# Kernel optimization log

Hardware: AMD Instinct MI355X
Metric: run time of the kernel (lower is better)

Reference implementation:

```python
import jax, jax.numpy as jnp
import numpy as np
from itertools import permutations

NB_OBJ = 3
DIM_BODY = 10
DIM_OBJECT = 15
OBJ_IDS = np.array([[0, 1, 2], [3, 4, 5], [6, 7, 8]])
LOG_SIG_MIN, LOG_SIG_MAX = -20.0, 2.0


def _lin(key, fan_in, fan_out):
    # torch nn.Linear default init: U(-1/sqrt(fan_in), 1/sqrt(fan_in))
    kw, kb = jax.random.split(key)
    lim = 1.0 / np.sqrt(fan_in)
    w = jax.random.uniform(kw, (fan_in, fan_out), jnp.float32, -lim, lim)
    b = jax.random.uniform(kb, (fan_out,), jnp.float32, -lim, lim)
    return w, b


def setup_inputs() -> dict:
    key = jax.random.key(0)
    ks = jax.random.split(key, 8)
    B = 65536
    d_phi_in, hid, d_phi_out, d_act = 58, 256, 256, 4

    obs = jax.random.normal(ks[0], (B, DIM_BODY + NB_OBJ * DIM_OBJECT), jnp.float32)
    ag = jax.random.normal(ks[1], (B, 9), jnp.float32)
    g = jax.random.normal(ks[2], (B, 9), jnp.float32)

    phi_w1, phi_b1 = _lin(ks[3], d_phi_in, hid)
    phi_w2, phi_b2 = _lin(ks[4], hid, d_phi_out)
    rho_w1, rho_b1 = _lin(ks[5], d_phi_out, 256)
    mean_w, mean_b = _lin(ks[6], 256, d_act)
    logstd_w, logstd_b = _lin(ks[7], 256, d_act)

    return {
        "obs": obs, "ag": ag, "g": g,
        "phi_w1": phi_w1, "phi_b1": phi_b1,
        "phi_w2": phi_w2, "phi_b2": phi_b2,
        "rho_w1": rho_w1, "rho_b1": rho_b1,
        "mean_w": mean_w, "mean_b": mean_b,
        "logstd_w": logstd_w, "logstd_b": logstd_b,
    }


def reference(obs, ag, g, phi_w1, phi_b1, phi_w2, phi_b2,
              rho_w1, rho_b1, mean_w, mean_b, logstd_w, logstd_b):
    B = obs.shape[0]
    obs_body = obs[:, :DIM_BODY]                       # [B, 10]
    eye = jnp.eye(NB_OBJ, dtype=obs.dtype)
    # obs_objects[i]: [B, 3 one-hot + 15 features]
    obs_objects = [
        jnp.concatenate(
            [jnp.broadcast_to(eye[i], (B, NB_OBJ)),
             obs[:, DIM_BODY + DIM_OBJECT * i: DIM_BODY + DIM_OBJECT * (i + 1)]],
            axis=1)
        for i in range(NB_OBJ)
    ]
    perms = list(permutations(range(NB_OBJ), 2))       # 6 ordered pairs
    # inp: [6, B, 58]
    inp = jnp.stack([
        jnp.concatenate([ag[:, OBJ_IDS[i]], ag[:, OBJ_IDS[j]],
                         g[:, OBJ_IDS[i]], g[:, OBJ_IDS[j]],
                         obs_body, obs_objects[i], obs_objects[j]], axis=1)
        for i, j in perms
    ])
    # shared phi MLP over all pairs
    h = jax.nn.relu(inp @ phi_w1 + phi_b1)             # [6, B, 256]
    phi_out = jax.nn.relu(h @ phi_w2 + phi_b2)         # [6, B, 256]
    pooled = phi_out.sum(axis=0)                       # [B, 256] sum-pool over pairs
    # rho MLP
    x = jax.nn.relu(pooled @ rho_w1 + rho_b1)          # [B, 256]
    mean = x @ mean_w + mean_b                         # [B, 4]
    logstd = jnp.clip(x @ logstd_w + logstd_b, LOG_SIG_MIN, LOG_SIG_MAX)
    return mean, logstd
```

## Files before the change

### kernel.cpp

```cpp
#include <hip/hip_runtime.h>


typedef __bf16 bf16x8 __attribute__((ext_vector_type(8)));
typedef float f32x4 __attribute__((ext_vector_type(4)));
typedef unsigned short u16x8 __attribute__((ext_vector_type(8)));

#define HB_OFF   0
#define INP0_OFF 32768
#define INP1_OFF 40960
#define RAW_OFF  49152
#define STAB_OFF 59648
#define LDS_TOTAL 60416

__device__ __forceinline__ unsigned short f2bf(float f) {
  union { float f; unsigned u; } v; v.f = f;
  unsigned r = v.u + 0x7fffu + ((v.u >> 16) & 1u);
  return (unsigned short)(r >> 16);
}
__device__ __forceinline__ int swz512(int o) { return o ^ (((o >> 9) & 7) << 4); }
__device__ __forceinline__ int swz128(int o) { return o ^ (((o >> 7) & 7) << 4); }
__device__ __forceinline__ f32x4 mfma16(bf16x8 a, bf16x8 b, f32x4 c) {
  return __builtin_amdgcn_mfma_f32_16x16x32_bf16(a, b, c, 0, 0, 0);
}
__device__ __forceinline__ uint2 pack4(f32x4 v) {
  uint2 r;
  asm("v_cvt_pk_bf16_f32 %0, %1, %2" : "=v"(r.x) : "v"(v[0]), "v"(v[1]));
  asm("v_cvt_pk_bf16_f32 %0, %1, %2" : "=v"(r.y) : "v"(v[2]), "v"(v[3]));
  return r;
}

__global__ void actor_prep(const float* __restrict__ w1, const float* __restrict__ w2,
                           const float* __restrict__ rho, const float* __restrict__ mw,
                           const float* __restrict__ lw, unsigned short* __restrict__ ws16) {
  int idx = blockIdx.x * blockDim.x + threadIdx.x;
  const int T = 16384 + 65536 + 65536 + 4096;
  for (; idx < T; idx += gridDim.x * blockDim.x) {
    float v;
    if (idx < 16384) {
      int n = idx >> 6, k = idx & 63;
      v = (k < 58) ? w1[k * 256 + n] : 0.f;
    } else if (idx < 81920) {
      int o = idx - 16384; int n = o >> 8, k = o & 255;
      v = w2[k * 256 + n];
    } else if (idx < 147456) {
      int o = idx - 81920; int n = o >> 8, k = o & 255;
      v = rho[k * 256 + n];
    } else {
      int o = idx - 147456; int n = o >> 8, k = o & 255;
      v = (n < 4) ? mw[k * 4 + n] : ((n < 8) ? lw[k * 4 + (n - 4)] : 0.f);
    }
    ws16[idx] = f2bf(v);
  }
}

__global__ __launch_bounds__(512, 1) void actor_main(
    const float* __restrict__ obs, const float* __restrict__ ag, const float* __restrict__ g,
    const float* __restrict__ b1v, const float* __restrict__ b2v, const float* __restrict__ rbv,
    const float* __restrict__ mbv, const float* __restrict__ lbv,
    const unsigned short* __restrict__ ws16,
    float* __restrict__ out, int B) {
  __shared__ char smem[LDS_TOTAL];
  unsigned short* rawp = (unsigned short*)(smem + RAW_OFF);
  unsigned short* stab = (unsigned short*)(smem + STAB_OFF);

  const unsigned short* w1t   = ws16;
  const unsigned short* w2t   = ws16 + 16384;
  const unsigned short* rhot  = ws16 + 81920;
  const unsigned short* headt = ws16 + 147456;

  const int tid = threadIdx.x;
  const int lane = tid & 63;
  const int wv = tid >> 6;
  const int l15 = lane & 15;
  const int lq = lane >> 4;
  const int wbase = wv * 32;
  const int ntiles = B / 64;
  const f32x4 fzero = {0.f, 0.f, 0.f, 0.f};

  bf16x8 wf2[8][2];
#pragma unroll
  for (int kk = 0; kk < 8; kk++)
#pragma unroll
    for (int nt = 0; nt < 2; nt++)
      wf2[kk][nt] = *(const bf16x8*)&w2t[(wbase + nt * 16 + l15) * 256 + kk * 32 + lq * 8];
  bf16x8 w1r[2][2];
#pragma unroll
  for (int nt = 0; nt < 2; nt++)
#pragma unroll
    for (int kk = 0; kk < 2; kk++)
      w1r[nt][kk] = *(const bf16x8*)&w1t[(wbase + nt * 16 + l15) * 64 + kk * 32 + lq * 8];
  f32x4 b1f[2], b2f[2], rbf[2];
#pragma unroll
  for (int nt = 0; nt < 2; nt++) {
    b1f[nt] = *(const f32x4*)&b1v[wbase + nt * 16 + lq * 4];
    b2f[nt] = *(const f32x4*)&b2v[wbase + nt * 16 + lq * 4];
    rbf[nt] = *(const f32x4*)&rbv[wbase + nt * 16 + lq * 4];
  }
  f32x4 mb4 = *(const f32x4*)mbv;
  f32x4 lb4 = *(const f32x4*)lbv;

  if (tid < 384) {
    const int PI[6] = {0, 0, 1, 1, 2, 2};
    const int PJ[6] = {1, 2, 0, 2, 0, 1};
    int p = tid >> 6, c = tid & 63;
    int pi = PI[p], pj = PJ[p], s;
    if (c < 3)       s = 56 + 3 * pi + c;
    else if (c < 6)  s = 56 + 3 * pj + (c - 3);
    else if (c < 9)  s = 65 + 3 * pi + (c - 6);
    else if (c < 12) s = 65 + 3 * pj + (c - 9);
    else if (c < 22) s = c - 12;
    else if (c < 25) s = ((c - 22) == pi) ? 75 : 74;
    else if (c < 40) s = 10 + 15 * pi + (c - 25);
    else if (c < 43) s = ((c - 40) == pj) ? 75 : 74;
    else if (c < 58) s = 10 + 15 * pj + (c - 43);
    else             s = 74;
    stab[tid] = (unsigned short)s;
  }

  for (int t = blockIdx.x; t < ntiles; t += gridDim.x) {
    const long brow = (long)t * 64;

    for (int i = tid; i < 64 * 55; i += 512) {
      int r = i / 55, c = i - r * 55;
      rawp[r * 82 + c] = f2bf(obs[brow * 55 + i]);
    }
    for (int i = tid; i < 64 * 9; i += 512) {
      int r = i / 9, c = i - r * 9;
      rawp[r * 82 + 56 + c] = f2bf(ag[brow * 9 + i]);
      rawp[r * 82 + 65 + c] = f2bf(g[brow * 9 + i]);
    }
    if (tid < 64) {
      rawp[tid * 82 + 55] = 0;
      rawp[tid * 82 + 74] = 0;
      rawp[tid * 82 + 75] = 0x3F80;
    }
    __syncthreads();

    {
      int r = tid >> 3, oct = tid & 7;
      u16x8 sv = *(const u16x8*)&stab[0 * 64 + oct * 8];
      const unsigned short* rw = &rawp[r * 82];
      uint4 w;
      w.x = (unsigned)rw[sv[0]] | ((unsigned)rw[sv[1]] << 16);
      w.y = (unsigned)rw[sv[2]] | ((unsigned)rw[sv[3]] << 16);
      w.z = (unsigned)rw[sv[4]] | ((unsigned)rw[sv[5]] << 16);
      w.w = (unsigned)rw[sv[6]] | ((unsigned)rw[sv[7]] << 16);
      *(uint4*)(smem + INP0_OFF + swz128(r * 128 + oct * 16)) = w;
    }
    __syncthreads();

    f32x4 pooled[2][4];
#pragma unroll
    for (int a = 0; a < 2; a++)
#pragma unroll
      for (int b = 0; b < 4; b++) pooled[a][b] = fzero;

    for (int p = 0; p < 6; p++) {
      const int ib = (p & 1) ? INP1_OFF : INP0_OFF;
      f32x4 acc1[2][4];
#pragma unroll
      for (int nt = 0; nt < 2; nt++)
#pragma unroll
        for (int mt = 0; mt < 4; mt++) acc1[nt][mt] = b1f[nt];
#pragma unroll
      for (int kk = 0; kk < 2; kk++) {
        bf16x8 xf[4];
#pragma unroll
        for (int mt = 0; mt < 4; mt++)
          xf[mt] = *(const bf16x8*)(smem + ib +
                     swz128((mt * 16 + l15) * 128 + (kk * 32 + lq * 8) * 2));
#pragma unroll
        for (int nt = 0; nt < 2; nt++)
#pragma unroll
          for (int mt = 0; mt < 4; mt++)
            acc1[nt][mt] = mfma16(w1r[nt][kk], xf[mt], acc1[nt][mt]);
      }
#pragma unroll
      for (int nt = 0; nt < 2; nt++)
#pragma unroll
        for (int mt = 0; mt < 4; mt++) {
          f32x4 h;
#pragma unroll
          for (int r = 0; r < 4; r++) h[r] = fmaxf(acc1[nt][mt][r], 0.f);
          *(uint2*)(smem + HB_OFF + swz512((mt * 16 + l15) * 512 +
                     (wbase + nt * 16 + lq * 4) * 2)) = pack4(h);
        }
      __syncthreads();

      if (p < 5) {
        int r = tid >> 3, oct = tid & 7;
        u16x8 sv = *(const u16x8*)&stab[(p + 1) * 64 + oct * 8];
        const unsigned short* rw = &rawp[r * 82];
        uint4 w;
        w.x = (unsigned)rw[sv[0]] | ((unsigned)rw[sv[1]] << 16);
        w.y = (unsigned)rw[sv[2]] | ((unsigned)rw[sv[3]] << 16);
        w.z = (unsigned)rw[sv[4]] | ((unsigned)rw[sv[5]] << 16);
        w.w = (unsigned)rw[sv[6]] | ((unsigned)rw[sv[7]] << 16);
        *(uint4*)(smem + ((p & 1) ? INP0_OFF : INP1_OFF) + swz128(r * 128 + oct * 16)) = w;
      }
      f32x4 acc2[2][4];
#pragma unroll
      for (int nt = 0; nt < 2; nt++)
#pragma unroll
        for (int mt = 0; mt < 4; mt++) acc2[nt][mt] = b2f[nt];
      __builtin_amdgcn_s_setprio(1);
#pragma unroll
      for (int kk = 0; kk < 8; kk++) {
        bf16x8 hf[4];
#pragma unroll
        for (int mt = 0; mt < 4; mt++)
          hf[mt] = *(const bf16x8*)(smem + HB_OFF +
                     swz512((mt * 16 + l15) * 512 + (kk * 32 + lq * 8) * 2));
#pragma unroll
        for (int nt = 0; nt < 2; nt++)
#pragma unroll
          for (int mt = 0; mt < 4; mt++)
            acc2[nt][mt] = mfma16(wf2[kk][nt], hf[mt], acc2[nt][mt]);
      }
      __builtin_amdgcn_s_setprio(0);
#pragma unroll
      for (int nt = 0; nt < 2; nt++)
#pragma unroll
        for (int mt = 0; mt < 4; mt++)
#pragma unroll
          for (int r = 0; r < 4; r++)
            pooled[nt][mt][r] += fmaxf(acc2[nt][mt][r], 0.f);
      __syncthreads();
    }

#pragma unroll
    for (int nt = 0; nt < 2; nt++)
#pragma unroll
      for (int mt = 0; mt < 4; mt++)
        *(uint2*)(smem + HB_OFF + swz512((mt * 16 + l15) * 512 +
                   (wbase + nt * 16 + lq * 4) * 2)) = pack4(pooled[nt][mt]);
    __syncthreads();

    f32x4 acc3[2][4];
#pragma unroll
    for (int nt = 0; nt < 2; nt++)
#pragma unroll
      for (int mt = 0; mt < 4; mt++) acc3[nt][mt] = rbf[nt];
#pragma unroll
    for (int kk = 0; kk < 8; kk++) {
      bf16x8 wf[2], hf[4];
#pragma unroll
      for (int nt = 0; nt < 2; nt++)
        wf[nt] = *(const bf16x8*)&rhot[(wbase + nt * 16 + l15) * 256 + kk * 32 + lq * 8];
#pragma unroll
      for (int mt = 0; mt < 4; mt++)
        hf[mt] = *(const bf16x8*)(smem + HB_OFF +
                   swz512((mt * 16 + l15) * 512 + (kk * 32 + lq * 8) * 2));
#pragma unroll
      for (int nt = 0; nt < 2; nt++)
#pragma unroll
        for (int mt = 0; mt < 4; mt++)
          acc3[nt][mt] = mfma16(wf[nt], hf[mt], acc3[nt][mt]);
    }
    __syncthreads();
#pragma unroll
    for (int nt = 0; nt < 2; nt++)
#pragma unroll
      for (int mt = 0; mt < 4; mt++) {
        f32x4 x;
#pragma unroll
        for (int r = 0; r < 4; r++) x[r] = fmaxf(acc3[nt][mt][r], 0.f);
        *(uint2*)(smem + HB_OFF + swz512((mt * 16 + l15) * 512 +
                   (wbase + nt * 16 + lq * 4) * 2)) = pack4(x);
      }
    __syncthreads();

    if (wv < 4) {
      f32x4 acc4 = fzero;
      if (lq == 0)      acc4 = mb4;
      else if (lq == 1) acc4 = lb4;
#pragma unroll
      for (int kk = 0; kk < 8; kk++) {
        bf16x8 hf = *(const bf16x8*)(smem + HB_OFF +
                      swz512((wv * 16 + l15) * 512 + (kk * 32 + lq * 8) * 2));
        bf16x8 wf = *(const bf16x8*)&headt[l15 * 256 + kk * 32 + lq * 8];
        acc4 = mfma16(wf, hf, acc4);
      }
      long gr = brow + wv * 16 + l15;
      if (lq == 0) {
        *(f32x4*)&out[gr * 4] = acc4;
      } else if (lq == 1) {
        f32x4 u;
#pragma unroll
        for (int r = 0; r < 4; r++) u[r] = fminf(fmaxf(acc4[r], -20.f), 2.f);
        *(f32x4*)&out[(long)B * 4 + gr * 4] = u;
      }
    }
  }
}

extern "C" void kernel_launch(void* const* d_in, const int* in_sizes, int n_in,
                              void* d_out, int out_size, void* d_ws, size_t ws_size,
                              hipStream_t stream) {
  const float* obs = (const float*)d_in[0];
  const float* ag  = (const float*)d_in[1];
  const float* g   = (const float*)d_in[2];
  const float* w1  = (const float*)d_in[3];
  const float* b1  = (const float*)d_in[4];
  const float* w2  = (const float*)d_in[5];
  const float* b2  = (const float*)d_in[6];
  const float* rw  = (const float*)d_in[7];
  const float* rb  = (const float*)d_in[8];
  const float* mw  = (const float*)d_in[9];
  const float* mb  = (const float*)d_in[10];
  const float* lw  = (const float*)d_in[11];
  const float* lb  = (const float*)d_in[12];
  int B = in_sizes[0] / 55;

  unsigned short* ws16 = (unsigned short*)d_ws;
  hipLaunchKernelGGL(actor_prep, dim3(128), dim3(256), 0, stream, w1, w2, rw, mw, lw, ws16);
  hipLaunchKernelGGL(actor_main, dim3(256), dim3(512), 0, stream,
                     obs, ag, g, b1, b2, rb, mb, lb, ws16, (float*)d_out, B);
}
```

Baseline: 112.8 us.

## Double block size to 1024 threads, each wave computing 16 output columns

Launches 1024-thread blocks and assigns each of 16 waves a 16-column slice of every layer instead of 32 columns per wave across 8 waves. This halves per-wave register state (weights, accumulators, pooled sums) and raises the number of resident waves to hide LDS and MFMA latency. The launch bounds request of 4 blocks per CU may force a very small register budget and cause spills, and barriers now synchronize twice as many waves.

```diff
diff --git a/kernel.cpp b/kernel.cpp
--- a/kernel.cpp
+++ b/kernel.cpp
@@ -53,7 +53,7 @@
   }
 }
 
-__global__ __launch_bounds__(512, 1) void actor_main(
+__global__ __launch_bounds__(1024, 4) void actor_main(
     const float* __restrict__ obs, const float* __restrict__ ag, const float* __restrict__ g,
     const float* __restrict__ b1v, const float* __restrict__ b2v, const float* __restrict__ rbv,
     const float* __restrict__ mbv, const float* __restrict__ lbv,
@@ -73,29 +73,21 @@
   const int wv = tid >> 6;
   const int l15 = lane & 15;
   const int lq = lane >> 4;
-  const int wbase = wv * 32;
+  const int wbase = wv * 16;
   const int ntiles = B / 64;
   const f32x4 fzero = {0.f, 0.f, 0.f, 0.f};
 
-  bf16x8 wf2[8][2];
+  bf16x8 wf2[8];
 #pragma unroll
   for (int kk = 0; kk < 8; kk++)
-#pragma unroll
-    for (int nt = 0; nt < 2; nt++)
-      wf2[kk][nt] = *(const bf16x8*)&w2t[(wbase + nt * 16 + l15) * 256 + kk * 32 + lq * 8];
-  bf16x8 w1r[2][2];
-#pragma unroll
-  for (int nt = 0; nt < 2; nt++)
-#pragma unroll
-    for (int kk = 0; kk < 2; kk++)
-      w1r[nt][kk] = *(const bf16x8*)&w1t[(wbase + nt * 16 + l15) * 64 + kk * 32 + lq * 8];
-  f32x4 b1f[2], b2f[2], rbf[2];
-#pragma unroll
-  for (int nt = 0; nt < 2; nt++) {
-    b1f[nt] = *(const f32x4*)&b1v[wbase + nt * 16 + lq * 4];
-    b2f[nt] = *(const f32x4*)&b2v[wbase + nt * 16 + lq * 4];
-    rbf[nt] = *(const f32x4*)&rbv[wbase + nt * 16 + lq * 4];
-  }
+    wf2[kk] = *(const bf16x8*)&w2t[(wbase + l15) * 256 + kk * 32 + lq * 8];
+  bf16x8 w1r[2];
+#pragma unroll
+  for (int kk = 0; kk < 2; kk++)
+    w1r[kk] = *(const bf16x8*)&w1t[(wbase + l15) * 64 + kk * 32 + lq * 8];
+  f32x4 b1f = *(const f32x4*)&b1v[wbase + lq * 4];
+  f32x4 b2f = *(const f32x4*)&b2v[wbase + lq * 4];
+  f32x4 rbf = *(const f32x4*)&rbv[wbase + lq * 4];
   f32x4 mb4 = *(const f32x4*)mbv;
   f32x4 lb4 = *(const f32x4*)lbv;
 
@@ -120,12 +112,12 @@
   for (int t = blockIdx.x; t < ntiles; t += gridDim.x) {
     const long brow = (long)t * 64;
 
-    for (int i = tid; i < 64 * 55; i += 512) {
+    for (int i = tid; i < 64 * 55; i += 1024) {
       int r = i / 55, c = i - r * 55;
       rawp[r * 82 + c] = f2bf(obs[brow * 55 + i]);
     }
-    for (int i = tid; i < 64 * 9; i += 512) {
-      int r = i / 9, c = i - r * 9;
+    if (tid < 64 * 9) {
+      int i = tid, r = i / 9, c = i - r * 9;
       rawp[r * 82 + 56 + c] = f2bf(ag[brow * 9 + i]);
       rawp[r * 82 + 65 + c] = f2bf(g[brow * 9 + i]);
     }
@@ -136,7 +128,7 @@
     }
     __syncthreads();
 
-    {
+    if (tid < 512) {
       int r = tid >> 3, oct = tid & 7;
       u16x8 sv = *(const u16x8*)&stab[0 * 64 + oct * 8];
       const unsigned short* rw = &rawp[r * 82];
@@ -149,19 +141,15 @@
     }
     __syncthreads();
 
-    f32x4 pooled[2][4];
-#pragma unroll
-    for (int a = 0; a < 2; a++)
-#pragma unroll
-      for (int b = 0; b < 4; b++) pooled[a][b] = fzero;
+    f32x4 pooled[4];
+#pragma unroll
+    for (int b = 0; b < 4; b++) pooled[b] = fzero;
 
     for (int p = 0; p < 6; p++) {
       const int ib = (p & 1) ? INP1_OFF : INP0_OFF;
-      f32x4 acc1[2][4];
-#pragma unroll
-      for (int nt = 0; nt < 2; nt++)
-#pragma unroll
-        for (int mt = 0; mt < 4; mt++) acc1[nt][mt] = b1f[nt];
+      f32x4 acc1[4];
+#pragma unroll
+      for (int mt = 0; mt < 4; mt++) acc1[mt] = b1f;
 #pragma unroll
       for (int kk = 0; kk < 2; kk++) {
         bf16x8 xf[4];
@@ -170,24 +158,20 @@
           xf[mt] = *(const bf16x8*)(smem + ib +
                      swz128((mt * 16 + l15) * 128 + (kk * 32 + lq * 8) * 2));
 #pragma unroll
-        for (int nt = 0; nt < 2; nt++)
-#pragma unroll
-          for (int mt = 0; mt < 4; mt++)
-            acc1[nt][mt] = mfma16(w1r[nt][kk], xf[mt], acc1[nt][mt]);
-      }
-#pragma unroll
-      for (int nt = 0; nt < 2; nt++)
-#pragma unroll
-        for (int mt = 0; mt < 4; mt++) {
-          f32x4 h;
-#pragma unroll
-          for (int r = 0; r < 4; r++) h[r] = fmaxf(acc1[nt][mt][r], 0.f);
-          *(uint2*)(smem + HB_OFF + swz512((mt * 16 + l15) * 512 +
-                     (wbase + nt * 16 + lq * 4) * 2)) = pack4(h);
-        }
+        for (int mt = 0; mt < 4; mt++)
+          acc1[mt] = mfma16(w1r[kk], xf[mt], acc1[mt]);
+      }
+#pragma unroll
+      for (int mt = 0; mt < 4; mt++) {
+        f32x4 h;
+#pragma unroll
+        for (int r = 0; r < 4; r++) h[r] = fmaxf(acc1[mt][r], 0.f);
+        *(uint2*)(smem + HB_OFF + swz512((mt * 16 + l15) * 512 +
+                   (wbase + lq * 4) * 2)) = pack4(h);
+      }
       __syncthreads();
 
-      if (p < 5) {
+      if (p < 5 && tid < 512) {
         int r = tid >> 3, oct = tid & 7;
         u16x8 sv = *(const u16x8*)&stab[(p + 1) * 64 + oct * 8];
         const unsigned short* rw = &rawp[r * 82];
@@ -198,11 +182,9 @@
         w.w = (unsigned)rw[sv[6]] | ((unsigned)rw[sv[7]] << 16);
         *(uint4*)(smem + ((p & 1) ? INP0_OFF : INP1_OFF) + swz128(r * 128 + oct * 16)) = w;
       }
-      f32x4 acc2[2][4];
-#pragma unroll
-      for (int nt = 0; nt < 2; nt++)
-#pragma unroll
-        for (int mt = 0; mt < 4; mt++) acc2[nt][mt] = b2f[nt];
+      f32x4 acc2[4];
+#pragma unroll
+      for (int mt = 0; mt < 4; mt++) acc2[mt] = b2f;
       __builtin_amdgcn_s_setprio(1);
 #pragma unroll
       for (int kk = 0; kk < 8; kk++) {
@@ -212,62 +194,48 @@
           hf[mt] = *(const bf16x8*)(smem + HB_OFF +
                      swz512((mt * 16 + l15) * 512 + (kk * 32 + lq * 8) * 2));
 #pragma unroll
-        for (int nt = 0; nt < 2; nt++)
-#pragma unroll
-          for (int mt = 0; mt < 4; mt++)
-            acc2[nt][mt] = mfma16(wf2[kk][nt], hf[mt], acc2[nt][mt]);
+        for (int mt = 0; mt < 4; mt++)
+          acc2[mt] = mfma16(wf2[kk], hf[mt], acc2[mt]);
       }
       __builtin_amdgcn_s_setprio(0);
 #pragma unroll
-      for (int nt = 0; nt < 2; nt++)
-#pragma unroll
-        for (int mt = 0; mt < 4; mt++)
-#pragma unroll
-          for (int r = 0; r < 4; r++)
-            pooled[nt][mt][r] += fmaxf(acc2[nt][mt][r], 0.f);
+      for (int mt = 0; mt < 4; mt++)
+#pragma unroll
+        for (int r = 0; r < 4; r++)
+          pooled[mt][r] += fmaxf(acc2[mt][r], 0.f);
       __syncthreads();
     }
 
 #pragma unroll
-    for (int nt = 0; nt < 2; nt++)
-#pragma unroll
-      for (int mt = 0; mt < 4; mt++)
-        *(uint2*)(smem + HB_OFF + swz512((mt * 16 + l15) * 512 +
-                   (wbase + nt * 16 + lq * 4) * 2)) = pack4(pooled[nt][mt]);
-    __syncthreads();
-
-    f32x4 acc3[2][4];
-#pragma unroll
-    for (int nt = 0; nt < 2; nt++)
-#pragma unroll
-      for (int mt = 0; mt < 4; mt++) acc3[nt][mt] = rbf[nt];
+    for (int mt = 0; mt < 4; mt++)
+      *(uint2*)(smem + HB_OFF + swz512((mt * 16 + l15) * 512 +
+                 (wbase + lq * 4) * 2)) = pack4(pooled[mt]);
+    __syncthreads();
+
+    f32x4 acc3[4];
+#pragma unroll
+    for (int mt = 0; mt < 4; mt++) acc3[mt] = rbf;
 #pragma unroll
     for (int kk = 0; kk < 8; kk++) {
-      bf16x8 wf[2], hf[4];
-#pragma unroll
-      for (int nt = 0; nt < 2; nt++)
-        wf[nt] = *(const bf16x8*)&rhot[(wbase + nt * 16 + l15) * 256 + kk * 32 + lq * 8];
+      bf16x8 wf = *(const bf16x8*)&rhot[(wbase + l15) * 256 + kk * 32 + lq * 8];
+      bf16x8 hf[4];
 #pragma unroll
       for (int mt = 0; mt < 4; mt++)
         hf[mt] = *(const bf16x8*)(smem + HB_OFF +
                    swz512((mt * 16 + l15) * 512 + (kk * 32 + lq * 8) * 2));
 #pragma unroll
-      for (int nt = 0; nt < 2; nt++)
-#pragma unroll
-        for (int mt = 0; mt < 4; mt++)
-          acc3[nt][mt] = mfma16(wf[nt], hf[mt], acc3[nt][mt]);
-    }
-    __syncthreads();
-#pragma unroll
-    for (int nt = 0; nt < 2; nt++)
-#pragma unroll
-      for (int mt = 0; mt < 4; mt++) {
-        f32x4 x;
-#pragma unroll
-        for (int r = 0; r < 4; r++) x[r] = fmaxf(acc3[nt][mt][r], 0.f);
-        *(uint2*)(smem + HB_OFF + swz512((mt * 16 + l15) * 512 +
-                   (wbase + nt * 16 + lq * 4) * 2)) = pack4(x);
-      }
+      for (int mt = 0; mt < 4; mt++)
+        acc3[mt] = mfma16(wf, hf[mt], acc3[mt]);
+    }
+    __syncthreads();
+#pragma unroll
+    for (int mt = 0; mt < 4; mt++) {
+      f32x4 x;
+#pragma unroll
+      for (int r = 0; r < 4; r++) x[r] = fmaxf(acc3[mt][r], 0.f);
+      *(uint2*)(smem + HB_OFF + swz512((mt * 16 + l15) * 512 +
+                 (wbase + lq * 4) * 2)) = pack4(x);
+    }
     __syncthreads();
 
     if (wv < 4) {
@@ -314,6 +282,6 @@
 
   unsigned short* ws16 = (unsigned short*)d_ws;
   hipLaunchKernelGGL(actor_prep, dim3(128), dim3(256), 0, stream, w1, w2, rw, mw, lw, ws16);
-  hipLaunchKernelGGL(actor_main, dim3(256), dim3(512), 0, stream,
+  hipLaunchKernelGGL(actor_main, dim3(256), dim3(1024), 0, stream,
                      obs, ag, g, b1, b2, rb, mb, lb, ws16, (float*)d_out, B);
 }
```

Result: slower. 176.3 us (+56.2%).

## Replace persistent 64-row tiling with one 32-row tile per 256-thread block

Applied to the files above, without the earlier changes.

The persistent kernel (256 blocks of 512 threads looping over 64-row tiles) becomes a one-shot grid of B/32 blocks, each with 4 waves handling 32 rows. Each wave now owns 64 output columns instead of 32, and LDS use is halved to allow more resident blocks per CU. The aim is more parallel blocks and better latency hiding. In exchange, every block reloads the full W2 register fragment, the bias vectors and the W1 and rho weights from global/L2. That greatly raises weight traffic and doubles the weight registers per wave.

```diff
diff --git a/kernel.cpp b/kernel.cpp
--- a/kernel.cpp
+++ b/kernel.cpp
@@ -6,11 +6,11 @@
 typedef unsigned short u16x8 __attribute__((ext_vector_type(8)));
 
 #define HB_OFF   0
-#define INP0_OFF 32768
-#define INP1_OFF 40960
-#define RAW_OFF  49152
-#define STAB_OFF 59648
-#define LDS_TOTAL 60416
+#define INP0_OFF 16384
+#define INP1_OFF 20480
+#define RAW_OFF  24576
+#define STAB_OFF 29824
+#define LDS_TOTAL 30592
 
 __device__ __forceinline__ unsigned short f2bf(float f) {
   union { float f; unsigned u; } v; v.f = f;
@@ -53,7 +53,7 @@
   }
 }
 
-__global__ __launch_bounds__(512, 1) void actor_main(
+__global__ __launch_bounds__(256, 1) void actor_main(
     const float* __restrict__ obs, const float* __restrict__ ag, const float* __restrict__ g,
     const float* __restrict__ b1v, const float* __restrict__ b2v, const float* __restrict__ rbv,
     const float* __restrict__ mbv, const float* __restrict__ lbv,
@@ -73,36 +73,21 @@
   const int wv = tid >> 6;
   const int l15 = lane & 15;
   const int lq = lane >> 4;
-  const int wbase = wv * 32;
-  const int ntiles = B / 64;
+  const int wbase = wv * 64;
+  const long brow = (long)blockIdx.x * 32;
   const f32x4 fzero = {0.f, 0.f, 0.f, 0.f};
 
-  bf16x8 wf2[8][2];
+  bf16x8 wf2[8][4];
 #pragma unroll
   for (int kk = 0; kk < 8; kk++)
 #pragma unroll
-    for (int nt = 0; nt < 2; nt++)
+    for (int nt = 0; nt < 4; nt++)
       wf2[kk][nt] = *(const bf16x8*)&w2t[(wbase + nt * 16 + l15) * 256 + kk * 32 + lq * 8];
-  bf16x8 w1r[2][2];
-#pragma unroll
-  for (int nt = 0; nt < 2; nt++)
-#pragma unroll
-    for (int kk = 0; kk < 2; kk++)
-      w1r[nt][kk] = *(const bf16x8*)&w1t[(wbase + nt * 16 + l15) * 64 + kk * 32 + lq * 8];
-  f32x4 b1f[2], b2f[2], rbf[2];
-#pragma unroll
-  for (int nt = 0; nt < 2; nt++) {
-    b1f[nt] = *(const f32x4*)&b1v[wbase + nt * 16 + lq * 4];
-    b2f[nt] = *(const f32x4*)&b2v[wbase + nt * 16 + lq * 4];
-    rbf[nt] = *(const f32x4*)&rbv[wbase + nt * 16 + lq * 4];
-  }
-  f32x4 mb4 = *(const f32x4*)mbv;
-  f32x4 lb4 = *(const f32x4*)lbv;
-
-  if (tid < 384) {
+
+  for (int i = tid; i < 384; i += 256) {
     const int PI[6] = {0, 0, 1, 1, 2, 2};
     const int PJ[6] = {1, 2, 0, 2, 0, 1};
-    int p = tid >> 6, c = tid & 63;
+    int p = i >> 6, c = i & 63;
     int pi = PI[p], pj = PJ[p], s;
     if (c < 3)       s = 56 + 3 * pi + c;
     else if (c < 6)  s = 56 + 3 * pj + (c - 3);
@@ -114,182 +99,184 @@
     else if (c < 43) s = ((c - 40) == pj) ? 75 : 74;
     else if (c < 58) s = 10 + 15 * pj + (c - 43);
     else             s = 74;
-    stab[tid] = (unsigned short)s;
-  }
-
-  for (int t = blockIdx.x; t < ntiles; t += gridDim.x) {
-    const long brow = (long)t * 64;
-
-    for (int i = tid; i < 64 * 55; i += 512) {
-      int r = i / 55, c = i - r * 55;
-      rawp[r * 82 + c] = f2bf(obs[brow * 55 + i]);
-    }
-    for (int i = tid; i < 64 * 9; i += 512) {
-      int r = i / 9, c = i - r * 9;
-      rawp[r * 82 + 56 + c] = f2bf(ag[brow * 9 + i]);
-      rawp[r * 82 + 65 + c] = f2bf(g[brow * 9 + i]);
-    }
-    if (tid < 64) {
-      rawp[tid * 82 + 55] = 0;
-      rawp[tid * 82 + 74] = 0;
-      rawp[tid * 82 + 75] = 0x3F80;
-    }
+    stab[i] = (unsigned short)s;
+  }
+
+  for (int i = tid; i < 32 * 55; i += 256) {
+    int r = i / 55, c = i - r * 55;
+    rawp[r * 82 + c] = f2bf(obs[brow * 55 + i]);
+  }
+  for (int i = tid; i < 32 * 9; i += 256) {
+    int r = i / 9, c = i - r * 9;
+    rawp[r * 82 + 56 + c] = f2bf(ag[brow * 9 + i]);
+    rawp[r * 82 + 65 + c] = f2bf(g[brow * 9 + i]);
+  }
+  if (tid < 32) {
+    rawp[tid * 82 + 55] = 0;
+    rawp[tid * 82 + 74] = 0;
+    rawp[tid * 82 + 75] = 0x3F80;
+  }
+  __syncthreads();
+
+  {
+    int r = tid >> 3, oct = tid & 7;
+    u16x8 sv = *(const u16x8*)&stab[0 * 64 + oct * 8];
+    const unsigned short* rw = &rawp[r * 82];
+    uint4 w;
+    w.x = (unsigned)rw[sv[0]] | ((unsigned)rw[sv[1]] << 16);
+    w.y = (unsigned)rw[sv[2]] | ((unsigned)rw[sv[3]] << 16);
+    w.z = (unsigned)rw[sv[4]] | ((unsigned)rw[sv[5]] << 16);
+    w.w = (unsigned)rw[sv[6]] | ((unsigned)rw[sv[7]] << 16);
+    *(uint4*)(smem + INP0_OFF + swz128(r * 128 + oct * 16)) = w;
+  }
+  __syncthreads();
+
+  f32x4 pooled[4][2];
+#pragma unroll
+  for (int a = 0; a < 4; a++)
+#pragma unroll
+    for (int b = 0; b < 2; b++) pooled[a][b] = fzero;
+
+  for (int p = 0; p < 6; p++) {
+    const int ib = (p & 1) ? INP1_OFF : INP0_OFF;
+    f32x4 acc1[4][2];
+#pragma unroll
+    for (int nt = 0; nt < 4; nt++) {
+      f32x4 b = *(const f32x4*)&b1v[wbase + nt * 16 + lq * 4];
+      acc1[nt][0] = b; acc1[nt][1] = b;
+    }
+#pragma unroll
+    for (int kk = 0; kk < 2; kk++) {
+      bf16x8 w1f[4], xf[2];
+#pragma unroll
+      for (int nt = 0; nt < 4; nt++)
+        w1f[nt] = *(const bf16x8*)&w1t[(wbase + nt * 16 + l15) * 64 + kk * 32 + lq * 8];
+#pragma unroll
+      for (int mt = 0; mt < 2; mt++)
+        xf[mt] = *(const bf16x8*)(smem + ib +
+                   swz128((mt * 16 + l15) * 128 + (kk * 32 + lq * 8) * 2));
+#pragma unroll
+      for (int nt = 0; nt < 4; nt++)
+#pragma unroll
+        for (int mt = 0; mt < 2; mt++)
+          acc1[nt][mt] = mfma16(w1f[nt], xf[mt], acc1[nt][mt]);
+    }
+#pragma unroll
+    for (int nt = 0; nt < 4; nt++)
+#pragma unroll
+      for (int mt = 0; mt < 2; mt++) {
+        f32x4 h;
+#pragma unroll
+        for (int r = 0; r < 4; r++) h[r] = fmaxf(acc1[nt][mt][r], 0.f);
+        *(uint2*)(smem + HB_OFF + swz512((mt * 16 + l15) * 512 +
+                   (wbase + nt * 16 + lq * 4) * 2)) = pack4(h);
+      }
     __syncthreads();
 
-    {
+    if (p < 5) {
       int r = tid >> 3, oct = tid & 7;
-      u16x8 sv = *(const u16x8*)&stab[0 * 64 + oct * 8];
+      u16x8 sv = *(const u16x8*)&stab[(p + 1) * 64 + oct * 8];
       const unsigned short* rw = &rawp[r * 82];
       uint4 w;
       w.x = (unsigned)rw[sv[0]] | ((unsigned)rw[sv[1]] << 16);
       w.y = (unsigned)rw[sv[2]] | ((unsigned)rw[sv[3]] << 16);
       w.z = (unsigned)rw[sv[4]] | ((unsigned)rw[sv[5]] << 16);
       w.w = (unsigned)rw[sv[6]] | ((unsigned)rw[sv[7]] << 16);
-      *(uint4*)(smem + INP0_OFF + swz128(r * 128 + oct * 16)) = w;
-    }
-    __syncthreads();
-
-    f32x4 pooled[2][4];
-#pragma unroll
-    for (int a = 0; a < 2; a++)
-#pragma unroll
-      for (int b = 0; b < 4; b++) pooled[a][b] = fzero;
-
-    for (int p = 0; p < 6; p++) {
-      const int ib = (p & 1) ? INP1_OFF : INP0_OFF;
-      f32x4 acc1[2][4];
-#pragma unroll
-      for (int nt = 0; nt < 2; nt++)
-#pragma unroll
-        for (int mt = 0; mt < 4; mt++) acc1[nt][mt] = b1f[nt];
-#pragma unroll
-      for (int kk = 0; kk < 2; kk++) {
-        bf16x8 xf[4];
-#pragma unroll
-        for (int mt = 0; mt < 4; mt++)
-          xf[mt] = *(const bf16x8*)(smem + ib +
-                     swz128((mt * 16 + l15) * 128 + (kk * 32 + lq * 8) * 2));
-#pragma unroll
-        for (int nt = 0; nt < 2; nt++)
-#pragma unroll
-          for (int mt = 0; mt < 4; mt++)
-            acc1[nt][mt] = mfma16(w1r[nt][kk], xf[mt], acc1[nt][mt]);
-      }
-#pragma unroll
-      for (int nt = 0; nt < 2; nt++)
-#pragma unroll
-        for (int mt = 0; mt < 4; mt++) {
-          f32x4 h;
-#pragma unroll
-          for (int r = 0; r < 4; r++) h[r] = fmaxf(acc1[nt][mt][r], 0.f);
-          *(uint2*)(smem + HB_OFF + swz512((mt * 16 + l15) * 512 +
-                     (wbase + nt * 16 + lq * 4) * 2)) = pack4(h);
-        }
-      __syncthreads();
-
-      if (p < 5) {
-        int r = tid >> 3, oct = tid & 7;
-        u16x8 sv = *(const u16x8*)&stab[(p + 1) * 64 + oct * 8];
-        const unsigned short* rw = &rawp[r * 82];
-        uint4 w;
-        w.x = (unsigned)rw[sv[0]] | ((unsigned)rw[sv[1]] << 16);
-        w.y = (unsigned)rw[sv[2]] | ((unsigned)rw[sv[3]] << 16);
-        w.z = (unsigned)rw[sv[4]] | ((unsigned)rw[sv[5]] << 16);
-        w.w = (unsigned)rw[sv[6]] | ((unsigned)rw[sv[7]] << 16);
-        *(uint4*)(smem + ((p & 1) ? INP0_OFF : INP1_OFF) + swz128(r * 128 + oct * 16)) = w;
-      }
-      f32x4 acc2[2][4];
-#pragma unroll
-      for (int nt = 0; nt < 2; nt++)
-#pragma unroll
-        for (int mt = 0; mt < 4; mt++) acc2[nt][mt] = b2f[nt];
-      __builtin_amdgcn_s_setprio(1);
-#pragma unroll
-      for (int kk = 0; kk < 8; kk++) {
-        bf16x8 hf[4];
-#pragma unroll
-        for (int mt = 0; mt < 4; mt++)
-          hf[mt] = *(const bf16x8*)(smem + HB_OFF +
-                     swz512((mt * 16 + l15) * 512 + (kk * 32 + lq * 8) * 2));
-#pragma unroll
-        for (int nt = 0; nt < 2; nt++)
-#pragma unroll
-          for (int mt = 0; mt < 4; mt++)
-            acc2[nt][mt] = mfma16(wf2[kk][nt], hf[mt], acc2[nt][mt]);
-      }
-      __builtin_amdgcn_s_setprio(0);
-#pragma unroll
-      for (int nt = 0; nt < 2; nt++)
-#pragma unroll
-        for (int mt = 0; mt < 4; mt++)
-#pragma unroll
-          for (int r = 0; r < 4; r++)
-            pooled[nt][mt][r] += fmaxf(acc2[nt][mt][r], 0.f);
-      __syncthreads();
-    }
-
-#pragma unroll
-    for (int nt = 0; nt < 2; nt++)
-#pragma unroll
-      for (int mt = 0; mt < 4; mt++)
-        *(uint2*)(smem + HB_OFF + swz512((mt * 16 + l15) * 512 +
-                   (wbase + nt * 16 + lq * 4) * 2)) = pack4(pooled[nt][mt]);
-    __syncthreads();
-
-    f32x4 acc3[2][4];
-#pragma unroll
-    for (int nt = 0; nt < 2; nt++)
-#pragma unroll
-      for (int mt = 0; mt < 4; mt++) acc3[nt][mt] = rbf[nt];
+      *(uint4*)(smem + ((p & 1) ? INP0_OFF : INP1_OFF) + swz128(r * 128 + oct * 16)) = w;
+    }
+    f32x4 acc2[4][2];
+#pragma unroll
+    for (int nt = 0; nt < 4; nt++) {
+      f32x4 b = *(const f32x4*)&b2v[wbase + nt * 16 + lq * 4];
+      acc2[nt][0] = b; acc2[nt][1] = b;
+    }
+    __builtin_amdgcn_s_setprio(1);
 #pragma unroll
     for (int kk = 0; kk < 8; kk++) {
-      bf16x8 wf[2], hf[4];
-#pragma unroll
-      for (int nt = 0; nt < 2; nt++)
-        wf[nt] = *(const bf16x8*)&rhot[(wbase + nt * 16 + l15) * 256 + kk * 32 + lq * 8];
-#pragma unroll
-      for (int mt = 0; mt < 4; mt++)
+      bf16x8 hf[2];
+#pragma unroll
+      for (int mt = 0; mt < 2; mt++)
         hf[mt] = *(const bf16x8*)(smem + HB_OFF +
                    swz512((mt * 16 + l15) * 512 + (kk * 32 + lq * 8) * 2));
 #pragma unroll
-      for (int nt = 0; nt < 2; nt++)
-#pragma unroll
-        for (int mt = 0; mt < 4; mt++)
-          acc3[nt][mt] = mfma16(wf[nt], hf[mt], acc3[nt][mt]);
-    }
+      for (int nt = 0; nt < 4; nt++)
+#pragma unroll
+        for (int mt = 0; mt < 2; mt++)
+          acc2[nt][mt] = mfma16(wf2[kk][nt], hf[mt], acc2[nt][mt]);
+    }
+    __builtin_amdgcn_s_setprio(0);
+#pragma unroll
+    for (int nt = 0; nt < 4; nt++)
+#pragma unroll
+      for (int mt = 0; mt < 2; mt++)
+#pragma unroll
+        for (int r = 0; r < 4; r++)
+          pooled[nt][mt][r] += fmaxf(acc2[nt][mt][r], 0.f);
     __syncthreads();
-#pragma unroll
-    for (int nt = 0; nt < 2; nt++)
-#pragma unroll
-      for (int mt = 0; mt < 4; mt++) {
-        f32x4 x;
-#pragma unroll
-        for (int r = 0; r < 4; r++) x[r] = fmaxf(acc3[nt][mt][r], 0.f);
-        *(uint2*)(smem + HB_OFF + swz512((mt * 16 + l15) * 512 +
-                   (wbase + nt * 16 + lq * 4) * 2)) = pack4(x);
-      }
-    __syncthreads();
-
-    if (wv < 4) {
-      f32x4 acc4 = fzero;
-      if (lq == 0)      acc4 = mb4;
-      else if (lq == 1) acc4 = lb4;
-#pragma unroll
-      for (int kk = 0; kk < 8; kk++) {
-        bf16x8 hf = *(const bf16x8*)(smem + HB_OFF +
-                      swz512((wv * 16 + l15) * 512 + (kk * 32 + lq * 8) * 2));
-        bf16x8 wf = *(const bf16x8*)&headt[l15 * 256 + kk * 32 + lq * 8];
-        acc4 = mfma16(wf, hf, acc4);
-      }
-      long gr = brow + wv * 16 + l15;
-      if (lq == 0) {
-        *(f32x4*)&out[gr * 4] = acc4;
-      } else if (lq == 1) {
-        f32x4 u;
-#pragma unroll
-        for (int r = 0; r < 4; r++) u[r] = fminf(fmaxf(acc4[r], -20.f), 2.f);
-        *(f32x4*)&out[(long)B * 4 + gr * 4] = u;
-      }
+  }
+
+#pragma unroll
+  for (int nt = 0; nt < 4; nt++)
+#pragma unroll
+    for (int mt = 0; mt < 2; mt++)
+      *(uint2*)(smem + HB_OFF + swz512((mt * 16 + l15) * 512 +
+                 (wbase + nt * 16 + lq * 4) * 2)) = pack4(pooled[nt][mt]);
+  __syncthreads();
+
+  f32x4 acc3[4][2];
+#pragma unroll
+  for (int nt = 0; nt < 4; nt++) {
+    f32x4 b = *(const f32x4*)&rbv[wbase + nt * 16 + lq * 4];
+    acc3[nt][0] = b; acc3[nt][1] = b;
+  }
+#pragma unroll
+  for (int kk = 0; kk < 8; kk++) {
+    bf16x8 wf[4], hf[2];
+#pragma unroll
+    for (int nt = 0; nt < 4; nt++)
+      wf[nt] = *(const bf16x8*)&rhot[(wbase + nt * 16 + l15) * 256 + kk * 32 + lq * 8];
+#pragma unroll
+    for (int mt = 0; mt < 2; mt++)
+      hf[mt] = *(const bf16x8*)(smem + HB_OFF +
+                 swz512((mt * 16 + l15) * 512 + (kk * 32 + lq * 8) * 2));
+#pragma unroll
+    for (int nt = 0; nt < 4; nt++)
+#pragma unroll
+      for (int mt = 0; mt < 2; mt++)
+        acc3[nt][mt] = mfma16(wf[nt], hf[mt], acc3[nt][mt]);
+  }
+  __syncthreads();
+#pragma unroll
+  for (int nt = 0; nt < 4; nt++)
+#pragma unroll
+    for (int mt = 0; mt < 2; mt++) {
+      f32x4 x;
+#pragma unroll
+      for (int r = 0; r < 4; r++) x[r] = fmaxf(acc3[nt][mt][r], 0.f);
+      *(uint2*)(smem + HB_OFF + swz512((mt * 16 + l15) * 512 +
+                 (wbase + nt * 16 + lq * 4) * 2)) = pack4(x);
+    }
+  __syncthreads();
+
+  if (wv < 2) {
+    f32x4 acc4 = fzero;
+    if (lq == 0)      acc4 = *(const f32x4*)mbv;
+    else if (lq == 1) acc4 = *(const f32x4*)lbv;
+#pragma unroll
+    for (int kk = 0; kk < 8; kk++) {
+      bf16x8 hf = *(const bf16x8*)(smem + HB_OFF +
+                    swz512((wv * 16 + l15) * 512 + (kk * 32 + lq * 8) * 2));
+      bf16x8 wf = *(const bf16x8*)&headt[l15 * 256 + kk * 32 + lq * 8];
+      acc4 = mfma16(wf, hf, acc4);
+    }
+    long gr = brow + wv * 16 + l15;
+    if (lq == 0) {
+      *(f32x4*)&out[gr * 4] = acc4;
+    } else if (lq == 1) {
+      f32x4 u;
+#pragma unroll
+      for (int r = 0; r < 4; r++) u[r] = fminf(fmaxf(acc4[r], -20.f), 2.f);
+      *(f32x4*)&out[(long)B * 4 + gr * 4] = u;
     }
   }
 }
@@ -314,6 +301,6 @@
 
   unsigned short* ws16 = (unsigned short*)d_ws;
   hipLaunchKernelGGL(actor_prep, dim3(128), dim3(256), 0, stream, w1, w2, rw, mw, lw, ws16);
-  hipLaunchKernelGGL(actor_main, dim3(256), dim3(512), 0, stream,
+  hipLaunchKernelGGL(actor_main, dim3(B / 32), dim3(256), 0, stream,
                      obs, ag, g, b1, b2, rb, mb, lb, ws16, (float*)d_out, B);
 }
```

Result: slower. 189.9 us (+68.3%).

## Park resident weights in AGPRs and raise occupancy to two blocks per CU

Applied to the files above, without the earlier changes.

Moves the register-resident phi weight fragments (w1 and w2) into accumulation registers using explicit v_accvgpr_write/read, and reloads biases from global memory per use instead of keeping them live. Launch bounds change from one to two 512-thread blocks per CU so more waves can hide latency. The cost is extra accvgpr_read instructions in the MFMA inner loops and repeated small bias loads. LDS use (~60KB per block) may limit how many blocks actually fit.

```diff
diff --git a/kernel.cpp b/kernel.cpp
--- a/kernel.cpp
+++ b/kernel.cpp
@@ -3,6 +3,7 @@
 
 typedef __bf16 bf16x8 __attribute__((ext_vector_type(8)));
 typedef float f32x4 __attribute__((ext_vector_type(4)));
+typedef int v4i __attribute__((ext_vector_type(4)));
 typedef unsigned short u16x8 __attribute__((ext_vector_type(8)));
 
 #define HB_OFF   0
@@ -28,6 +29,14 @@
   asm("v_cvt_pk_bf16_f32 %0, %1, %2" : "=v"(r.y) : "v"(v[2]), "v"(v[3]));
   return r;
 }
+#define AG_WRITE(dst, w)                                                    \
+  {                                                                         \
+    asm volatile("v_accvgpr_write_b32 %0, %1" : "=a"((dst)[0]) : "v"((w)[0])); \
+    asm volatile("v_accvgpr_write_b32 %0, %1" : "=a"((dst)[1]) : "v"((w)[1])); \
+    asm volatile("v_accvgpr_write_b32 %0, %1" : "=a"((dst)[2]) : "v"((w)[2])); \
+    asm volatile("v_accvgpr_read_b32 %0, %1" : "=v"((w)[0]) : "a"((dst)[0])); \
+  }
+#undef AG_WRITE
 
 __global__ void actor_prep(const float* __restrict__ w1, const float* __restrict__ w2,
                            const float* __restrict__ rho, const float* __restrict__ mw,
@@ -53,7 +62,7 @@
   }
 }
 
-__global__ __launch_bounds__(512, 1) void actor_main(
+__global__ __launch_bounds__(512, 2) void actor_main(
     const float* __restrict__ obs, const float* __restrict__ ag, const float* __restrict__ g,
     const float* __restrict__ b1v, const float* __restrict__ b2v, const float* __restrict__ rbv,
     const float* __restrict__ mbv, const float* __restrict__ lbv,
@@ -77,27 +86,28 @@
   const int ntiles = B / 64;
   const f32x4 fzero = {0.f, 0.f, 0.f, 0.f};
 
-  bf16x8 wf2[8][2];
+  int wf2a[8][2][4];
 #pragma unroll
   for (int kk = 0; kk < 8; kk++)
 #pragma unroll
-    for (int nt = 0; nt < 2; nt++)
-      wf2[kk][nt] = *(const bf16x8*)&w2t[(wbase + nt * 16 + l15) * 256 + kk * 32 + lq * 8];
-  bf16x8 w1r[2][2];
+    for (int nt = 0; nt < 2; nt++) {
+      v4i w = *(const v4i*)&w2t[(wbase + nt * 16 + l15) * 256 + kk * 32 + lq * 8];
+#pragma unroll
+      for (int d = 0; d < 4; d++)
+        asm volatile("v_accvgpr_write_b32 %0, %1"
+                     : "=a"(wf2a[kk][nt][d]) : "v"(w[d]));
+    }
+  int w1a[2][2][4];
 #pragma unroll
   for (int nt = 0; nt < 2; nt++)
 #pragma unroll
-    for (int kk = 0; kk < 2; kk++)
-      w1r[nt][kk] = *(const bf16x8*)&w1t[(wbase + nt * 16 + l15) * 64 + kk * 32 + lq * 8];
-  f32x4 b1f[2], b2f[2], rbf[2];
-#pragma unroll
-  for (int nt = 0; nt < 2; nt++) {
-    b1f[nt] = *(const f32x4*)&b1v[wbase + nt * 16 + lq * 4];
-    b2f[nt] = *(const f32x4*)&b2v[wbase + nt * 16 + lq * 4];
-    rbf[nt] = *(const f32x4*)&rbv[wbase + nt * 16 + lq * 4];
-  }
-  f32x4 mb4 = *(const f32x4*)mbv;
-  f32x4 lb4 = *(const f32x4*)lbv;
+    for (int kk = 0; kk < 2; kk++) {
+      v4i w = *(const v4i*)&w1t[(wbase + nt * 16 + l15) * 64 + kk * 32 + lq * 8];
+#pragma unroll
+      for (int d = 0; d < 4; d++)
+        asm volatile("v_accvgpr_write_b32 %0, %1"
+                     : "=a"(w1a[nt][kk][d]) : "v"(w[d]));
+    }
 
   if (tid < 384) {
     const int PI[6] = {0, 0, 1, 1, 2, 2};
@@ -159,9 +169,11 @@
       const int ib = (p & 1) ? INP1_OFF : INP0_OFF;
       f32x4 acc1[2][4];
 #pragma unroll
-      for (int nt = 0; nt < 2; nt++)
-#pragma unroll
-        for (int mt = 0; mt < 4; mt++) acc1[nt][mt] = b1f[nt];
+      for (int nt = 0; nt < 2; nt++) {
+        f32x4 b = *(const f32x4*)&b1v[wbase + nt * 16 + lq * 4];
+#pragma unroll
+        for (int mt = 0; mt < 4; mt++) acc1[nt][mt] = b;
+      }
 #pragma unroll
       for (int kk = 0; kk < 2; kk++) {
         bf16x8 xf[4];
@@ -170,10 +182,17 @@
           xf[mt] = *(const bf16x8*)(smem + ib +
                      swz128((mt * 16 + l15) * 128 + (kk * 32 + lq * 8) * 2));
 #pragma unroll
-        for (int nt = 0; nt < 2; nt++)
+        for (int nt = 0; nt < 2; nt++) {
+          v4i w;
+#pragma unroll
+          for (int d = 0; d < 4; d++)
+            asm volatile("v_accvgpr_read_b32 %0, %1"
+                         : "=v"(w[d]) : "a"(w1a[nt][kk][d]));
+          bf16x8 wf = *(bf16x8*)&w;
 #pragma unroll
           for (int mt = 0; mt < 4; mt++)
-            acc1[nt][mt] = mfma16(w1r[nt][kk], xf[mt], acc1[nt][mt]);
+            acc1[nt][mt] = mfma16(wf, xf[mt], acc1[nt][mt]);
+        }
       }
 #pragma unroll
       for (int nt = 0; nt < 2; nt++)
@@ -200,9 +219,11 @@
       }
       f32x4 acc2[2][4];
 #pragma unroll
-      for (int nt = 0; nt < 2; nt++)
-#pragma unroll
-        for (int mt = 0; mt < 4; mt++) acc2[nt][mt] = b2f[nt];
+      for (int nt = 0; nt < 2; nt++) {
+        f32x4 b = *(const f32x4*)&b2v[wbase + nt * 16 + lq * 4];
+#pragma unroll
+        for (int mt = 0; mt < 4; mt++) acc2[nt][mt] = b;
+      }
       __builtin_amdgcn_s_setprio(1);
 #pragma unroll
       for (int kk = 0; kk < 8; kk++) {
@@ -212,10 +233,17 @@
           hf[mt] = *(const bf16x8*)(smem + HB_OFF +
                      swz512((mt * 16 + l15) * 512 + (kk * 32 + lq * 8) * 2));
 #pragma unroll
-        for (int nt = 0; nt < 2; nt++)
+        for (int nt = 0; nt < 2; nt++) {
+          v4i w;
+#pragma unroll
+          for (int d = 0; d < 4; d++)
+            asm volatile("v_accvgpr_read_b32 %0, %1"
+                         : "=v"(w[d]) : "a"(wf2a[kk][nt][d]));
+          bf16x8 wf = *(bf16x8*)&w;
 #pragma unroll
           for (int mt = 0; mt < 4; mt++)
-            acc2[nt][mt] = mfma16(wf2[kk][nt], hf[mt], acc2[nt][mt]);
+            acc2[nt][mt] = mfma16(wf, hf[mt], acc2[nt][mt]);
+        }
       }
       __builtin_amdgcn_s_setprio(0);
 #pragma unroll
@@ -238,9 +266,11 @@
 
     f32x4 acc3[2][4];
 #pragma unroll
-    for (int nt = 0; nt < 2; nt++)
-#pragma unroll
-      for (int mt = 0; mt < 4; mt++) acc3[nt][mt] = rbf[nt];
+    for (int nt = 0; nt < 2; nt++) {
+      f32x4 b = *(const f32x4*)&rbv[wbase + nt * 16 + lq * 4];
+#pragma unroll
+      for (int mt = 0; mt < 4; mt++) acc3[nt][mt] = b;
+    }
 #pragma unroll
     for (int kk = 0; kk < 8; kk++) {
       bf16x8 wf[2], hf[4];
@@ -272,8 +302,8 @@
 
     if (wv < 4) {
       f32x4 acc4 = fzero;
-      if (lq == 0)      acc4 = mb4;
-      else if (lq == 1) acc4 = lb4;
+      if (lq == 0)      acc4 = *(const f32x4*)mbv;
+      else if (lq == 1) acc4 = *(const f32x4*)lbv;
 #pragma unroll
       for (int kk = 0; kk < 8; kk++) {
         bf16x8 hf = *(const bf16x8*)(smem + HB_OFF +
```

Result: slower. 124.6 us (+10.4%).
